# Kernel optimization log

Measured on AMD Instinct MI355X. Metric: run time of the kernel, lower is better.

## Reference

```python
import math
import jax, jax.numpy as jnp
import numpy as np

TAU = 2.0
THR = 1.0
ALPHA = 10.0

T, B, IN_DIM, OUT_DIM = 64, 128, 2048, 2048


def setup_inputs() -> dict:
    key = jax.random.key(0)
    k1, k2, k3 = jax.random.split(key, 3)
    x_seq = jax.random.normal(k1, (T, B, IN_DIM), dtype=jnp.float32)
    # scale like nn.Linear default init so membrane potentials are O(1)
    W = jax.random.normal(k2, (OUT_DIM, IN_DIM), dtype=jnp.float32) / math.sqrt(IN_DIM)
    b = jax.random.normal(k3, (OUT_DIM,), dtype=jnp.float32) * 0.01
    return {"x_seq": x_seq, "W": W, "b": b}


def spike(x):
    # forward: hard threshold (surrogate gradient only matters in bwd)
    return (x > 0).astype(x.dtype)


def reference(x_seq, W, b):
    decay = math.exp(-1.0 / TAU)
    # hoist the linear layer out of the recurrence: one big GEMM
    cur_seq = jnp.einsum("tbi,oi->tbo", x_seq, W) + b  # (T, B, OUT_DIM)
    mem0 = jnp.zeros((x_seq.shape[1], W.shape[0]), dtype=x_seq.dtype)

    def step(mem, cur):
        mem = mem * decay + cur
        spk = spike(mem - THR)
        mem = mem - spk * THR
        return mem, spk

    _, spk_seq = jax.lax.scan(step, mem0, cur_seq)
    return spk_seq  # (T, B, OUT_DIM)
```

## Files before the change

kernel.cpp:

```cpp
#include <hip/hip_runtime.h>
#include <hip/hip_bf16.h>
#include <math.h>


typedef unsigned short u16;
typedef __attribute__((ext_vector_type(8))) short bf16x8;
typedef __attribute__((ext_vector_type(4))) float f32x4;

constexpr int T_STEPS = 64;
constexpr int BATCH   = 128;
constexpr int K_DIM   = 2048;
constexpr int N_DIM   = 2048;
constexpr int M_DIM   = T_STEPS * BATCH;
constexpr int NCHAIN  = BATCH * N_DIM;

constexpr float DECAY_F32 = (float)0.6065306597126334;
constexpr float BAND      = 5e-4f;

#define GLDS16(g, l) __builtin_amdgcn_global_load_lds(                       \
    (const __attribute__((address_space(1))) void*)(g),                      \
    (__attribute__((address_space(3))) void*)(l), 16, 0, 0)

__global__ __launch_bounds__(256)
void split_bf16(const float* __restrict__ X, const float* __restrict__ W,
                u16* __restrict__ Ah, u16* __restrict__ Al,
                u16* __restrict__ Wh, u16* __restrict__ Wl,
                unsigned int* __restrict__ counters) {
    if (blockIdx.x == 0 && threadIdx.x < 128) counters[threadIdx.x] = 0u;

    constexpr int NA4 = (M_DIM * K_DIM) / 4;
    constexpr int NW4 = (N_DIM * K_DIM) / 4;
    const int i = blockIdx.x * 256 + threadIdx.x;
    const float* src; u16* dh; u16* dl; int base;
    if (i < NA4)            { src = X; dh = Ah; dl = Al; base = i; }
    else if (i < NA4 + NW4) { src = W; dh = Wh; dl = Wl; base = i - NA4; }
    else return;

    const float4 v = *(const float4*)(src + (size_t)base * 4);
    const float f[4] = {v.x, v.y, v.z, v.w};
    unsigned int hp[2], lp[2];
#pragma unroll
    for (int q = 0; q < 4; q += 2) {
        u16 hh[2], ll[2];
#pragma unroll
        for (int e = 0; e < 2; e++) {
            __hip_bfloat16 hb = __float2bfloat16(f[q + e]);
            const float hf = __bfloat162float(hb);
            __hip_bfloat16 lb = __float2bfloat16(f[q + e] - hf);
            hh[e] = *(u16*)&hb;
            ll[e] = *(u16*)&lb;
        }
        hp[q >> 1] = (unsigned int)hh[0] | ((unsigned int)hh[1] << 16);
        lp[q >> 1] = (unsigned int)ll[0] | ((unsigned int)ll[1] << 16);
    }
    *(uint2*)(dh + (size_t)base * 4) = make_uint2(hp[0], hp[1]);
    *(uint2*)(dl + (size_t)base * 4) = make_uint2(lp[0], lp[1]);
}

__global__ __launch_bounds__(512, 2)
void gemm_bf16x3q(const u16* __restrict__ Ah, const u16* __restrict__ Al,
                  const u16* __restrict__ Bh, const u16* __restrict__ Bl,
                  const float* __restrict__ bias, float* __restrict__ C) {
    extern __shared__ __align__(16) u16 smem[];
    u16* const sAh = smem;
    u16* const sAl = smem + 3 * 8192;
    u16* const sBh = smem + 6 * 8192;
    u16* const sBl = smem + 6 * 8192 + 3 * 4096;

    const int tid  = threadIdx.x;
    const int m0   = blockIdx.y * 256;
    const int n0   = blockIdx.x * 128;
    const int lane = tid & 63;
    const int wave = tid >> 6;
    const int wm   = wave >> 1;
    const int wn   = wave & 1;

    const int cA0 = tid, cA1 = tid + 512, cB0 = tid;
#define OFFA(c) ((size_t)(m0 + ((c) >> 6) * 16 + ((c) & 15)) * K_DIM + (((c) >> 4) & 3) * 8)
#define OFFB(c) ((size_t)(n0 + ((c) >> 6) * 16 + ((c) & 15)) * K_DIM + (((c) >> 4) & 3) * 8)
    const size_t a0 = OFFA(cA0), a1 = OFFA(cA1), b0 = OFFB(cB0);
#undef OFFA
#undef OFFB

    const int lA0 = wave * 512;
    const int lA1 = 4096 + wave * 512;
    const int lB0 = wave * 512;

    f32x4 acc[4][4];
#pragma unroll
    for (int i = 0; i < 4; i++)
#pragma unroll
        for (int j = 0; j < 4; j++) acc[i][j] = (f32x4){0.f, 0.f, 0.f, 0.f};

    bf16x8 fahA[4], falA[4], fbhA[4], fblA[4];
    bf16x8 fahB[4], falB[4], fbhB[4], fblB[4];

#define STAGE(s, kc) do {                                                    \
        const int kn_ = (kc) * 32;                                           \
        const int sA_ = (s) * 8192, sB_ = (s) * 4096;                        \
        GLDS16(Ah + a0 + kn_, sAh + sA_ + lA0);                              \
        GLDS16(Ah + a1 + kn_, sAh + sA_ + lA1);                              \
        GLDS16(Al + a0 + kn_, sAl + sA_ + lA0);                              \
        GLDS16(Al + a1 + kn_, sAl + sA_ + lA1);                              \
        GLDS16(Bh + b0 + kn_, sBh + sB_ + lB0);                              \
        GLDS16(Bl + b0 + kn_, sBl + sB_ + lB0);                              \
    } while (0)

#define LOADF(SET, s) do {                                                   \
        const int sA_ = (s) * 8192, sB_ = (s) * 4096;                        \
        _Pragma("unroll")                                                    \
        for (int ti = 0; ti < 4; ti++) {                                     \
            const int ta = wm * 4 + ti;                                      \
            fah##SET[ti] = *(const bf16x8*)&sAh[sA_ + (ta * 64 + lane) * 8]; \
            fal##SET[ti] = *(const bf16x8*)&sAl[sA_ + (ta * 64 + lane) * 8]; \
        }                                                                    \
        _Pragma("unroll")                                                    \
        for (int tj = 0; tj < 4; tj++) {                                     \
            const int tb = wn * 4 + tj;                                      \
            fbh##SET[tj] = *(const bf16x8*)&sBh[sB_ + (tb * 64 + lane) * 8]; \
            fbl##SET[tj] = *(const bf16x8*)&sBl[sB_ + (tb * 64 + lane) * 8]; \
        }                                                                    \
    } while (0)

#define COMPUTE(SET) do {                                                    \
        __builtin_amdgcn_s_setprio(1);                                       \
        _Pragma("unroll")                                                    \
        for (int ti = 0; ti < 4; ti++)                                       \
        _Pragma("unroll")                                                    \
        for (int tj = 0; tj < 4; tj++) {                                     \
            acc[ti][tj] = __builtin_amdgcn_mfma_f32_16x16x32_bf16(           \
                fah##SET[ti], fbh##SET[tj], acc[ti][tj], 0, 0, 0);           \
            acc[ti][tj] = __builtin_amdgcn_mfma_f32_16x16x32_bf16(           \
                fah##SET[ti], fbl##SET[tj], acc[ti][tj], 0, 0, 0);           \
            acc[ti][tj] = __builtin_amdgcn_mfma_f32_16x16x32_bf16(           \
                fal##SET[ti], fbh##SET[tj], acc[ti][tj], 0, 0, 0);           \
        }                                                                    \
        __builtin_amdgcn_s_setprio(0);                                       \
    } while (0)

#define WAITSYNC(vm) do {                                                    \
        asm volatile("s_waitcnt vmcnt(" #vm ") lgkmcnt(0)" ::: "memory");    \
        __builtin_amdgcn_sched_barrier(0);                                   \
        __builtin_amdgcn_s_barrier();                                        \
        __builtin_amdgcn_sched_barrier(0);                                   \
    } while (0)

    STAGE(0, 0);
    STAGE(1, 1);
    STAGE(2, 2);
    WAITSYNC(12);
    LOADF(A, 0);

    int s1 = 1, sW = 0;
    for (int kc = 0; kc < 62; kc += 2) {
        WAITSYNC(6);
        LOADF(B, s1);
        if (kc + 3 < 64) STAGE(sW, kc + 3);
        COMPUTE(A);
        s1 = (s1 == 2) ? 0 : s1 + 1;
        sW = (sW == 2) ? 0 : sW + 1;
        WAITSYNC(6);
        LOADF(A, s1);
        if (kc + 4 < 64) STAGE(sW, kc + 4);
        COMPUTE(B);
        s1 = (s1 == 2) ? 0 : s1 + 1;
        sW = (sW == 2) ? 0 : sW + 1;
    }
    WAITSYNC(0);
    LOADF(B, s1);
    COMPUTE(A);
    COMPUTE(B);

#undef WAITSYNC
#undef COMPUTE
#undef LOADF
#undef STAGE

#pragma unroll
    for (int tj = 0; tj < 4; tj++) {
        const int n  = n0 + wn * 64 + tj * 16 + (lane & 15);
        const float bv = bias[n];
#pragma unroll
        for (int ti = 0; ti < 4; ti++) {
            const int mbase = m0 + wm * 64 + ti * 16 + (lane >> 4) * 4;
#pragma unroll
            for (int r = 0; r < 4; r++)
                C[(size_t)(mbase + r) * N_DIM + n] = acc[ti][tj][r] + bv;
        }
    }
}

__global__ __launch_bounds__(256)
void lif_scan_band(float* __restrict__ buf, unsigned int* __restrict__ counters,
                   unsigned int* __restrict__ worklist) {
    const int idx = blockIdx.x * 256 + threadIdx.x;
    float mem = 0.0f;
    bool flag = false;
#pragma unroll
    for (int t = 0; t < T_STEPS; t++) {
        const size_t off = (size_t)t * NCHAIN + idx;
        mem = __fadd_rn(__fmul_rn(mem, DECAY_F32), buf[off]);
        const float d = __fsub_rn(mem, 1.0f);
        const bool spk = d > 0.0f;
        if (fabsf(d) < BAND) flag = true;
        buf[off] = spk ? 1.0f : 0.0f;
        if (spk) mem = __fsub_rn(mem, 1.0f);
    }
    if (flag) {
        const int b = idx >> 11, o = idx & 2047;
        const unsigned int p = atomicAdd(&counters[b], 1u);
        worklist[b * 2048 + p] = (unsigned int)o;
    }
}

#define RG 16
#define RJ 4
#define BKR 64

__global__ __launch_bounds__(256)
void lif_repair2(const float* __restrict__ X, const float* __restrict__ W,
                 const float* __restrict__ bias,
                 const unsigned int* __restrict__ counters,
                 const unsigned int* __restrict__ worklist,
                 float* __restrict__ out) {
    __shared__ float sX[BKR][T_STEPS + 1];
    __shared__ float sW[RG][BKR + 1];
    __shared__ float scur[T_STEPS][RG + 1];
    __shared__ float sspk[T_STEPS][RG + 1];
    __shared__ int   so[RG];

    const int b = blockIdx.x / RJ;
    const int j = blockIdx.x % RJ;
    const unsigned int n_b = counters[b];
    if (n_b == 0) return;
    const int ngroups = (int)(n_b + RG - 1) / RG;

    const int tid = threadIdx.x;
    const int t   = tid & 63;
    const int oi  = tid >> 6;

    for (int g = j; g < ngroups; g += RJ) {
        if (tid < RG) {
            const int slot = g * RG + tid;
            so[tid] = (slot < (int)n_b) ? (int)worklist[b * 2048 + slot] : -1;
        }
        __syncthreads();

        float Csum[4] = {0.f, 0.f, 0.f, 0.f};
        float P[4]    = {0.f, 0.f, 0.f, 0.f};

        for (int c = 0; c < K_DIM / BKR; c++) {
            if (c > 0 && (c % 5) == 0) {
#pragma unroll
                for (int q = 0; q < 4; q++) {
                    Csum[q] = __fadd_rn(Csum[q], P[q]);
                    P[q] = 0.f;
                }
            }
            const int k0 = c * BKR;
            {
                const int ts = tid >> 2;
                const int kq = (tid & 3) * 16;
                const float* src = &X[(size_t)(ts * BATCH + b) * K_DIM + k0 + kq];
#pragma unroll
                for (int q = 0; q < 4; q++) {
                    const float4 v = *(const float4*)(src + q * 4);
                    sX[kq + q * 4 + 0][ts] = v.x;
                    sX[kq + q * 4 + 1][ts] = v.y;
                    sX[kq + q * 4 + 2][ts] = v.z;
                    sX[kq + q * 4 + 3][ts] = v.w;
                }
            }
            {
                const int wo  = tid >> 4;
                const int wkq = (tid & 15) * 4;
                const int o   = so[wo];
                float4 v = {0.f, 0.f, 0.f, 0.f};
                if (o >= 0) v = *(const float4*)&W[(size_t)o * K_DIM + k0 + wkq];
                sW[wo][wkq + 0] = v.x; sW[wo][wkq + 1] = v.y;
                sW[wo][wkq + 2] = v.z; sW[wo][wkq + 3] = v.w;
            }
            __syncthreads();
#pragma unroll 8
            for (int k = 0; k < BKR; k++) {
                const float xv = sX[k][t];
#pragma unroll
                for (int q = 0; q < 4; q++)
                    P[q] = fmaf(xv, sW[oi * 4 + q][k], P[q]);
            }
            __syncthreads();
        }
#pragma unroll
        for (int q = 0; q < 4; q++) {
            Csum[q] = __fadd_rn(Csum[q], P[q]);
            const int o = so[oi * 4 + q];
            scur[t][oi * 4 + q] = (o >= 0) ? __fadd_rn(Csum[q], bias[o]) : 0.f;
        }
        __syncthreads();
        if (tid < RG && so[tid] >= 0) {
            float mem = 0.0f;
            for (int tt = 0; tt < T_STEPS; tt++) {
                mem = __fadd_rn(__fmul_rn(mem, DECAY_F32), scur[tt][tid]);
                const float d = __fsub_rn(mem, 1.0f);
                const bool spk = d > 0.0f;
                sspk[tt][tid] = spk ? 1.0f : 0.0f;
                if (spk) mem = __fsub_rn(mem, 1.0f);
            }
        }
        __syncthreads();
#pragma unroll
        for (int q = 0; q < 4; q++) {
            const int o = so[oi * 4 + q];
            if (o >= 0)
                out[(size_t)t * NCHAIN + (size_t)b * N_DIM + o] = sspk[t][oi * 4 + q];
        }
        __syncthreads();
    }
}

__global__ __launch_bounds__(256)
void lif_openblas_q320(const float* __restrict__ X, const float* __restrict__ W,
                       const float* __restrict__ bias, float* __restrict__ out) {
    __shared__ float As[16][T_STEPS + 4];
    __shared__ float Ws[16][64 + 4];
    __shared__ float curbuf[T_STEPS][64 + 1];
    const int tid = threadIdx.x;
    const int o0 = blockIdx.x * 64, b0 = blockIdx.y;
    const int tm = (tid & 15) * 4, tn = (tid >> 4) * 4;
    float Csum[4][4], Pacc[4][4];
#pragma unroll
    for (int i = 0; i < 4; i++)
#pragma unroll
        for (int j = 0; j < 4; j++) { Csum[i][j] = 0.f; Pacc[i][j] = 0.f; }
    for (int c = 0; c < K_DIM / 16; c++) {
        if (c > 0 && (c % 20) == 0) {
#pragma unroll
            for (int i = 0; i < 4; i++)
#pragma unroll
                for (int j = 0; j < 4; j++) {
                    Csum[i][j] = __fadd_rn(Csum[i][j], Pacc[i][j]);
                    Pacc[i][j] = 0.f;
                }
        }
        const int k0 = c * 16;
        {
            const int t = tid >> 2, kq = (tid & 3) * 4;
            const float4 av = *(const float4*)&X[(size_t)(t * BATCH + b0) * K_DIM + k0 + kq];
            As[kq + 0][t] = av.x; As[kq + 1][t] = av.y;
            As[kq + 2][t] = av.z; As[kq + 3][t] = av.w;
            const float4 wv = *(const float4*)&W[(size_t)(o0 + t) * K_DIM + k0 + kq];
            Ws[kq + 0][t] = wv.x; Ws[kq + 1][t] = wv.y;
            Ws[kq + 2][t] = wv.z; Ws[kq + 3][t] = wv.w;
        }
        __syncthreads();
#pragma unroll
        for (int k = 0; k < 16; k++) {
            float a[4], w[4];
#pragma unroll
            for (int i = 0; i < 4; i++) a[i] = As[k][tm + i];
#pragma unroll
            for (int j = 0; j < 4; j++) w[j] = Ws[k][tn + j];
#pragma unroll
            for (int i = 0; i < 4; i++)
#pragma unroll
                for (int j = 0; j < 4; j++) Pacc[i][j] = fmaf(a[i], w[j], Pacc[i][j]);
        }
        __syncthreads();
    }
#pragma unroll
    for (int i = 0; i < 4; i++)
#pragma unroll
        for (int j = 0; j < 4; j++)
            curbuf[tm + i][tn + j] =
                __fadd_rn(__fadd_rn(Csum[i][j], Pacc[i][j]), bias[o0 + tn + j]);
    __syncthreads();
    if (tid < 64) {
        float mem = 0.0f;
#pragma unroll
        for (int t = 0; t < T_STEPS; t++) {
            mem = __fadd_rn(__fmul_rn(mem, DECAY_F32), curbuf[t][tid]);
            const float d = __fsub_rn(mem, 1.0f);
            const bool spk = d > 0.0f;
            out[(size_t)t * NCHAIN + (size_t)b0 * N_DIM + o0 + tid] = spk ? 1.0f : 0.0f;
            if (spk) mem = __fsub_rn(mem, 1.0f);
        }
    }
}

extern "C" void kernel_launch(void* const* d_in, const int* in_sizes, int n_in,
                              void* d_out, int out_size, void* d_ws, size_t ws_size,
                              hipStream_t stream) {
    const float* x = nullptr; const float* W = nullptr; const float* bias = nullptr;
    for (int i = 0; i < n_in; i++) {
        if      (in_sizes[i] == M_DIM * K_DIM) x    = (const float*)d_in[i];
        else if (in_sizes[i] == N_DIM * K_DIM) W    = (const float*)d_in[i];
        else if (in_sizes[i] == N_DIM)         bias = (const float*)d_in[i];
    }
    if (!x)    x    = (const float*)d_in[0];
    if (!W)    W    = (const float*)d_in[1];
    if (!bias) bias = (const float*)d_in[2];
    float* out = (float*)d_out;

    const size_t off_cnt = 0;
    const size_t off_wl  = 512;
    const size_t off_Ah  = off_wl + (size_t)128 * 2048 * 4;
    const size_t szA     = (size_t)M_DIM * K_DIM * 2;
    const size_t szW     = (size_t)N_DIM * K_DIM * 2;
    const size_t off_Al  = off_Ah + szA;
    const size_t off_Wh  = off_Al + szA;
    const size_t off_Wl  = off_Wh + szW;
    const size_t need    = off_Wl + szW;

    if (ws_size < need) {
        dim3 grid(N_DIM / 64, BATCH);
        lif_openblas_q320<<<grid, 256, 0, stream>>>(x, W, bias, out);
        return;
    }

    char* ws = (char*)d_ws;
    unsigned int* counters = (unsigned int*)(ws + off_cnt);
    unsigned int* worklist = (unsigned int*)(ws + off_wl);
    u16* Ah = (u16*)(ws + off_Ah);
    u16* Al = (u16*)(ws + off_Al);
    u16* Wh = (u16*)(ws + off_Wh);
    u16* Wl = (u16*)(ws + off_Wl);

    split_bf16<<<(M_DIM * K_DIM / 4 + N_DIM * K_DIM / 4) / 256, 256, 0, stream>>>(
        x, W, Ah, Al, Wh, Wl, counters);
    dim3 ggrid(N_DIM / 128, M_DIM / 256);
    gemm_bf16x3q<<<ggrid, 512, 147456, stream>>>(Ah, Al, Wh, Wl, bias, out);
    lif_scan_band<<<NCHAIN / 256, 256, 0, stream>>>(out, counters, worklist);
    lif_repair2<<<128 * RJ, 256, 0, stream>>>(x, W, bias, counters, worklist, out);
}
```

Measured before the change: 472.2 us.

## Load A fragments directly from global to registers, stage only B in LDS

The GEMM stops staging the A (activation) tiles through LDS. Each wave now loads its A hi/lo fragments straight from global memory into registers one k-step ahead, and only B goes through the triple-buffered LDS pipeline. This cuts LDS use from 144KB to 48KB and removes the LDS write/read traffic for A. In exchange, global loads of A are duplicated across the two wn waves, and the loads sit in registers with less latency hiding.

```diff
diff --git a/kernel.cpp b/kernel.cpp
--- a/kernel.cpp
+++ b/kernel.cpp
@@ -58,14 +58,12 @@
 }
 
 __global__ __launch_bounds__(512, 2)
-void gemm_bf16x3q(const u16* __restrict__ Ah, const u16* __restrict__ Al,
+void gemm_bf16x3r(const u16* __restrict__ Ah, const u16* __restrict__ Al,
                   const u16* __restrict__ Bh, const u16* __restrict__ Bl,
                   const float* __restrict__ bias, float* __restrict__ C) {
     extern __shared__ __align__(16) u16 smem[];
-    u16* const sAh = smem;
-    u16* const sAl = smem + 3 * 8192;
-    u16* const sBh = smem + 6 * 8192;
-    u16* const sBl = smem + 6 * 8192 + 3 * 4096;
+    u16* const sBh = smem;
+    u16* const sBl = smem + 3 * 4096;
 
     const int tid  = threadIdx.x;
     const int m0   = blockIdx.y * 256;
@@ -75,16 +73,19 @@
     const int wm   = wave >> 1;
     const int wn   = wave & 1;
 
-    const int cA0 = tid, cA1 = tid + 512, cB0 = tid;
-#define OFFA(c) ((size_t)(m0 + ((c) >> 6) * 16 + ((c) & 15)) * K_DIM + (((c) >> 4) & 3) * 8)
-#define OFFB(c) ((size_t)(n0 + ((c) >> 6) * 16 + ((c) & 15)) * K_DIM + (((c) >> 4) & 3) * 8)
-    const size_t a0 = OFFA(cA0), a1 = OFFA(cA1), b0 = OFFB(cB0);
-#undef OFFA
-#undef OFFB
-
-    const int lA0 = wave * 512;
-    const int lA1 = 4096 + wave * 512;
+    const size_t b0 =
+        (size_t)(n0 + (tid >> 6) * 16 + (tid & 15)) * K_DIM + ((tid >> 4) & 3) * 8;
     const int lB0 = wave * 512;
+
+    const u16* pAh[4];
+    const u16* pAl[4];
+#pragma unroll
+    for (int ti = 0; ti < 4; ti++) {
+        const size_t off =
+            (size_t)(m0 + wm * 64 + ti * 16 + (lane & 15)) * K_DIM + (lane >> 4) * 8;
+        pAh[ti] = Ah + off;
+        pAl[ti] = Al + off;
+    }
 
     f32x4 acc[4][4];
 #pragma unroll
@@ -95,25 +96,23 @@
     bf16x8 fahA[4], falA[4], fbhA[4], fblA[4];
     bf16x8 fahB[4], falB[4], fbhB[4], fblB[4];
 
-#define STAGE(s, kc) do {                                                    \
+#define STAGEB(s, kc) do {                                                   \
         const int kn_ = (kc) * 32;                                           \
-        const int sA_ = (s) * 8192, sB_ = (s) * 4096;                        \
-        GLDS16(Ah + a0 + kn_, sAh + sA_ + lA0);                              \
-        GLDS16(Ah + a1 + kn_, sAh + sA_ + lA1);                              \
-        GLDS16(Al + a0 + kn_, sAl + sA_ + lA0);                              \
-        GLDS16(Al + a1 + kn_, sAl + sA_ + lA1);                              \
-        GLDS16(Bh + b0 + kn_, sBh + sB_ + lB0);                              \
-        GLDS16(Bl + b0 + kn_, sBl + sB_ + lB0);                              \
+        GLDS16(Bh + b0 + kn_, sBh + (s) * 4096 + lB0);                       \
+        GLDS16(Bl + b0 + kn_, sBl + (s) * 4096 + lB0);                       \
     } while (0)
 
-#define LOADF(SET, s) do {                                                   \
-        const int sA_ = (s) * 8192, sB_ = (s) * 4096;                        \
+#define LOADA(SET, kc) do {                                                  \
+        const int ko_ = (kc) * 32;                                           \
         _Pragma("unroll")                                                    \
         for (int ti = 0; ti < 4; ti++) {                                     \
-            const int ta = wm * 4 + ti;                                      \
-            fah##SET[ti] = *(const bf16x8*)&sAh[sA_ + (ta * 64 + lane) * 8]; \
-            fal##SET[ti] = *(const bf16x8*)&sAl[sA_ + (ta * 64 + lane) * 8]; \
+            fah##SET[ti] = *(const bf16x8*)(pAh[ti] + ko_);                  \
+            fal##SET[ti] = *(const bf16x8*)(pAl[ti] + ko_);                  \
         }                                                                    \
+    } while (0)
+
+#define LOADFB(SET, s) do {                                                  \
+        const int sB_ = (s) * 4096;                                          \
         _Pragma("unroll")                                                    \
         for (int tj = 0; tj < 4; tj++) {                                     \
             const int tb = wn * 4 + tj;                                      \
@@ -145,36 +144,48 @@
         __builtin_amdgcn_sched_barrier(0);                                   \
     } while (0)
 
-    STAGE(0, 0);
-    STAGE(1, 1);
-    STAGE(2, 2);
-    WAITSYNC(12);
-    LOADF(A, 0);
+#define FENCE __builtin_amdgcn_sched_barrier(0)
+
+    LOADA(A, 0);
+    STAGEB(0, 0);
+    STAGEB(1, 1);
+    STAGEB(2, 2);
+    WAITSYNC(4);
+    LOADFB(A, 0);
 
     int s1 = 1, sW = 0;
     for (int kc = 0; kc < 62; kc += 2) {
-        WAITSYNC(6);
-        LOADF(B, s1);
-        if (kc + 3 < 64) STAGE(sW, kc + 3);
+        WAITSYNC(2);
+        LOADA(B, kc + 1);
+        LOADFB(B, s1);
+        if (kc + 3 < 64) STAGEB(sW, kc + 3);
+        FENCE;
         COMPUTE(A);
         s1 = (s1 == 2) ? 0 : s1 + 1;
         sW = (sW == 2) ? 0 : sW + 1;
-        WAITSYNC(6);
-        LOADF(A, s1);
-        if (kc + 4 < 64) STAGE(sW, kc + 4);
+        WAITSYNC(2);
+        LOADA(A, kc + 2);
+        LOADFB(A, s1);
+        if (kc + 4 < 64) STAGEB(sW, kc + 4);
+        FENCE;
         COMPUTE(B);
         s1 = (s1 == 2) ? 0 : s1 + 1;
         sW = (sW == 2) ? 0 : sW + 1;
     }
     WAITSYNC(0);
-    LOADF(B, s1);
+    LOADA(B, 63);
+    LOADFB(B, 0);
+    FENCE;
     COMPUTE(A);
+    WAITSYNC(0);
     COMPUTE(B);
 
+#undef FENCE
 #undef WAITSYNC
 #undef COMPUTE
-#undef LOADF
-#undef STAGE
+#undef LOADFB
+#undef LOADA
+#undef STAGEB
 
 #pragma unroll
     for (int tj = 0; tj < 4; tj++) {
@@ -428,7 +439,7 @@
     split_bf16<<<(M_DIM * K_DIM / 4 + N_DIM * K_DIM / 4) / 256, 256, 0, stream>>>(
         x, W, Ah, Al, Wh, Wl, counters);
     dim3 ggrid(N_DIM / 128, M_DIM / 256);
-    gemm_bf16x3q<<<ggrid, 512, 147456, stream>>>(Ah, Al, Wh, Wl, bias, out);
+    gemm_bf16x3r<<<ggrid, 512, 49152, stream>>>(Ah, Al, Wh, Wl, bias, out);
     lif_scan_band<<<NCHAIN / 256, 256, 0, stream>>>(out, counters, worklist);
     lif_repair2<<<128 * RJ, 256, 0, stream>>>(x, W, bias, counters, worklist, out);
 }
```

Result: slower. 623.8 us (+32.1%).
